# Performance work log

Measured on AMD Instinct MI355X. Metric: run time of the kernel, lower is better.

Reference implementation:

```python
import jax, jax.numpy as jnp
import numpy as np

DIM = 128  # matches init kwarg `dim`; scale = 1/sqrt(dim)


def setup_inputs() -> dict:
    key = jax.random.key(0)
    kq, kk, kv = jax.random.split(key, 3)
    B, S, D = 16, 2048, 128
    return {
        "query": jax.random.normal(kq, (B, S, D), dtype=jnp.float32),
        "key": jax.random.normal(kk, (B, S, D), dtype=jnp.float32),
        "value": jax.random.normal(kv, (B, S, D), dtype=jnp.float32),
    }


def reference(query, key, value):
    # scores = Q K^T / sqrt(dim)  -> [B, S, S]
    scale = 1.0 / np.sqrt(DIM).astype(np.float32)
    scores = jnp.einsum("bqd,bkd->bqk", query, key) * scale
    attn = jax.nn.softmax(scores, axis=-1)
    # context = attn @ V -> [B, S, D]
    return jnp.einsum("bqk,bkd->bqd", attn, value)
```

## Files before the change

kernel.cpp:

```cpp
#include <hip/hip_runtime.h>
#include <hip/hip_bf16.h>

namespace {

constexpr int kS  = 2048;
constexpr int kD  = 128;
constexpr int kKB = 128;
constexpr int kNT = kS / kKB;
constexpr int kChunks = 2048;
constexpr size_t kImgUShorts = (size_t)16 * 16 * kChunks * 8;

typedef __attribute__((ext_vector_type(8)))  short bf16x8;
typedef __attribute__((ext_vector_type(16))) float f32x16;
typedef __attribute__((ext_vector_type(4)))  unsigned int u32x4;

__device__ inline unsigned short f2bf(float f) {
  return __builtin_bit_cast(unsigned short, __float2bfloat16(f));
}
__device__ inline unsigned pk2(float lo, float hi) {
  return (unsigned)f2bf(lo) | ((unsigned)f2bf(hi) << 16);
}
__device__ inline float fexp2(float x) { return __builtin_amdgcn_exp2f(x); }

__device__ inline void gload_lds16(const void* g, void* l) {
  __builtin_amdgcn_global_load_lds(
      (const __attribute__((address_space(1))) unsigned int*)g,
      (__attribute__((address_space(3))) unsigned int*)l, 16, 0, 0);
}

__global__ __launch_bounds__(256)
void convert_kv(const float* __restrict__ K, const float* __restrict__ V,
                unsigned short* __restrict__ Kws, unsigned short* __restrict__ Vws)
{
  const int tid = threadIdx.x;
  const int gid = blockIdx.x & 255;
  const int b = gid >> 4, t = gid & 15;
  if (blockIdx.x < 256) {
    const float* src = K + ((size_t)b * kS + t * kKB) * kD;
    unsigned short* dst = Kws + (size_t)gid * kChunks * 8;
#pragma unroll
    for (int i = 0; i < 8; ++i) {
      const int CH = i * 256 + tid;
      const int k = CH >> 4, s = CH & 15;
      const int d8 = s ^ (k & 15);
      const float* p = src + (size_t)k * kD + d8 * 8;
      float4 a = *reinterpret_cast<const float4*>(p);
      float4 c = *reinterpret_cast<const float4*>(p + 4);
      bf16x8 o;
      o[0] = (short)f2bf(a.x); o[1] = (short)f2bf(a.y);
      o[2] = (short)f2bf(a.z); o[3] = (short)f2bf(a.w);
      o[4] = (short)f2bf(c.x); o[5] = (short)f2bf(c.y);
      o[6] = (short)f2bf(c.z); o[7] = (short)f2bf(c.w);
      *reinterpret_cast<bf16x8*>(dst + (size_t)CH * 8) = o;
    }
  } else {
    __shared__ unsigned short VT[128 * 136];
    const float* src = V + ((size_t)b * kS + t * kKB) * kD;
#pragma unroll
    for (int i = 0; i < 16; ++i) {
      const int idx = i * 256 + tid;
      const int k = idx >> 5, d4 = idx & 31;
      float4 v = *reinterpret_cast<const float4*>(src + (size_t)k * kD + d4 * 4);
      VT[(d4 * 4 + 0) * 136 + k] = f2bf(v.x);
      VT[(d4 * 4 + 1) * 136 + k] = f2bf(v.y);
      VT[(d4 * 4 + 2) * 136 + k] = f2bf(v.z);
      VT[(d4 * 4 + 3) * 136 + k] = f2bf(v.w);
    }
    __syncthreads();
    unsigned short* dst = Vws + (size_t)gid * kChunks * 8;
#pragma unroll
    for (int i = 0; i < 8; ++i) {
      const int CH = i * 256 + tid;
      const int d = CH >> 4, s = CH & 15;
      const int k8 = s ^ (d & 15);
      bf16x8 v = *reinterpret_cast<const bf16x8*>(&VT[d * 136 + k8 * 8]);
      *reinterpret_cast<bf16x8*>(dst + (size_t)CH * 8) = v;
    }
  }
}

__global__ __launch_bounds__(512, 2)
void attn_fwd(const float* __restrict__ Q,
              const unsigned short* __restrict__ Kws,
              const unsigned short* __restrict__ Vws,
              float* __restrict__ O)
{
  __shared__ __align__(16) unsigned char smem[131072];
  __shared__ float mls[4 * 2 * 32];

  const int tid  = threadIdx.x;
  const int wv   = tid >> 6;
  const int qg   = wv & 3;
  const int ksp  = wv >> 2;
  const int lane = tid & 63;
  const int l31  = lane & 31;
  const int hi   = lane >> 5;
  const int m15  = l31 & 15;

  const int bid   = blockIdx.x;
  const int xcd   = bid & 7;
  const int slot  = bid >> 3;
  const int batch = xcd * 2 + (slot >> 4);
  const int qtile = slot & 15;

  const float* Qb = Q + (size_t)batch * kS * kD;
  float*       Ob = O + (size_t)batch * kS * kD;
  const int qrow0 = qtile * 128 + qg * 32;

  auto stageK = [&](int t, int buf) {
    const size_t base = ((size_t)(batch * 16 + t) * kChunks + wv * 256 + lane) * 8;
    unsigned char* kd = smem + buf * 32768 + wv * 4096;
    gload_lds16(Kws + base,           kd);
    gload_lds16(Kws + base + 64 * 8,  kd + 1024);
    gload_lds16(Kws + base + 128 * 8, kd + 2048);
    gload_lds16(Kws + base + 192 * 8, kd + 3072);
  };
  auto stageV = [&](int t, int buf) {
    const size_t base = ((size_t)(batch * 16 + t) * kChunks + wv * 256 + lane) * 8;
    unsigned char* vd = smem + 65536 + buf * 32768 + wv * 4096;
    gload_lds16(Vws + base,           vd);
    gload_lds16(Vws + base + 64 * 8,  vd + 1024);
    gload_lds16(Vws + base + 128 * 8, vd + 2048);
    gload_lds16(Vws + base + 192 * 8, vd + 3072);
  };

  stageK(0, 0); stageV(0, 0); stageK(1, 1);

  constexpr float kQScale = 0.08838834764831845f * 1.4426950408889634f;
  bf16x8 qf[8];
#pragma unroll
  for (int c = 0; c < 8; ++c) {
    const float* p = Qb + (size_t)(qrow0 + l31) * kD + c * 16 + hi * 8;
    float4 a = *reinterpret_cast<const float4*>(p);
    float4 b = *reinterpret_cast<const float4*>(p + 4);
    bf16x8 f;
    f[0] = (short)f2bf(a.x * kQScale); f[1] = (short)f2bf(a.y * kQScale);
    f[2] = (short)f2bf(a.z * kQScale); f[3] = (short)f2bf(a.w * kQScale);
    f[4] = (short)f2bf(b.x * kQScale); f[5] = (short)f2bf(b.y * kQScale);
    f[6] = (short)f2bf(b.z * kQScale); f[7] = (short)f2bf(b.w * kQScale);
    qf[c] = f;
  }

  f32x16 acc[4];
#pragma unroll
  for (int dt = 0; dt < 4; ++dt)
#pragma unroll
    for (int r = 0; r < 16; ++r) acc[dt][r] = 0.f;
  float mrun = -1e30f, lrun = 0.f;
  bf16x8 pa[2][2];

  __syncthreads();

  const unsigned short* Ksm = reinterpret_cast<const unsigned short*>(smem);
  const unsigned short* Vsm = reinterpret_cast<const unsigned short*>(smem + 65536);

  auto qk = [&](int kb, f32x16 sc[2]) {
#pragma unroll
    for (int kt = 0; kt < 2; ++kt)
#pragma unroll
      for (int r = 0; r < 16; ++r) sc[kt][r] = 0.f;
    __builtin_amdgcn_s_setprio(1);
#pragma unroll
    for (int c = 0; c < 8; ++c) {
      const int s = ((c << 1) | hi) ^ m15;
#pragma unroll
      for (int kt = 0; kt < 2; ++kt) {
        const int row = ksp * 64 + kt * 32 + l31;
        bf16x8 kf = *reinterpret_cast<const bf16x8*>(&Ksm[kb * 16384 + row * 128 + s * 8]);
        sc[kt] = __builtin_amdgcn_mfma_f32_32x32x16_bf16(kf, qf[c], sc[kt], 0, 0, 0);
      }
    }
    __builtin_amdgcn_s_setprio(0);
  };
  auto treemax = [&](const f32x16 sc[2]) {
    float m0 = sc[0][0];
#pragma unroll
    for (int r = 1; r < 16; ++r) m0 = fmaxf(m0, sc[0][r]);
#pragma unroll
    for (int r = 0; r < 16; ++r) m0 = fmaxf(m0, sc[1][r]);
    return fmaxf(m0, __shfl_xor(m0, 32));
  };
  auto pv = [&](int vb) {
    __builtin_amdgcn_s_setprio(1);
#pragma unroll
    for (int dt = 0; dt < 4; ++dt) {
      const int vRow = vb * 16384 + (dt * 32 + l31) * 128;
#pragma unroll
      for (int kt = 0; kt < 2; ++kt)
#pragma unroll
        for (int ks = 0; ks < 2; ++ks) {
          const int o = 8 * ksp + 4 * kt + 2 * ks + hi;
          bf16x8 vf = *reinterpret_cast<const bf16x8*>(&Vsm[vRow + (o ^ m15) * 8]);
          acc[dt] = __builtin_amdgcn_mfma_f32_32x32x16_bf16(vf, pa[kt][ks], acc[dt], 0, 0, 0);
        }
    }
    __builtin_amdgcn_s_setprio(0);
  };
  auto pack = [&](const f32x16& p, bf16x8* out) {
    unsigned a0 = pk2(p[0], p[1]),   a1 = pk2(p[2],  p[3]);
    unsigned a2 = pk2(p[4], p[5]),   a3 = pk2(p[6],  p[7]);
    unsigned b0 = pk2(p[8], p[9]),   b1 = pk2(p[10], p[11]);
    unsigned b2 = pk2(p[12], p[13]), b3 = pk2(p[14], p[15]);
    asm("v_permlane32_swap_b32 %0, %1" : "+v"(a0), "+v"(a2));
    asm("v_permlane32_swap_b32 %0, %1" : "+v"(a1), "+v"(a3));
    asm("v_permlane32_swap_b32 %0, %1" : "+v"(b0), "+v"(b2));
    asm("v_permlane32_swap_b32 %0, %1" : "+v"(b1), "+v"(b3));
    u32x4 w0 = {a0, a1, a2, a3};
    u32x4 w1 = {b0, b1, b2, b3};
    out[0] = __builtin_bit_cast(bf16x8, w0);
    out[1] = __builtin_bit_cast(bf16x8, w1);
  };

  {
    f32x16 sc[2];
    qk(0, sc);
    mrun = treemax(sc);
    float rs = 0.f;
#pragma unroll
    for (int kt = 0; kt < 2; ++kt)
#pragma unroll
      for (int r = 0; r < 16; ++r) { sc[kt][r] = fexp2(sc[kt][r] - mrun); rs += sc[kt][r]; }
    rs += __shfl_xor(rs, 32);
    lrun = rs;
    pack(sc[0], pa[0]);
    pack(sc[1], pa[1]);
  }
  __syncthreads();

  for (int t = 0; t < kNT - 1; ++t) {
    const int kb = (t + 1) & 1, vb = t & 1;
    if (t + 2 < kNT) stageK(t + 2, vb);
    stageV(t + 1, kb);

    f32x16 sc[2];
    qk(kb, sc);
    const float mt = treemax(sc);
    const bool need = !__all(mt - mrun <= 8.0f);
    const float mnew = need ? fmaxf(mrun, mt) : mrun;

    pv(vb);

    float rs = 0.f;
#pragma unroll
    for (int kt = 0; kt < 2; ++kt)
#pragma unroll
      for (int r = 0; r < 16; ++r) { sc[kt][r] = fexp2(sc[kt][r] - mnew); rs += sc[kt][r]; }
    rs += __shfl_xor(rs, 32);
    if (need) {
      const float corr = fexp2(mrun - mnew);
      lrun *= corr;
#pragma unroll
      for (int dt = 0; dt < 4; ++dt)
#pragma unroll
        for (int r = 0; r < 16; ++r) acc[dt][r] *= corr;
    }
    lrun += rs;
    mrun = mnew;
    pack(sc[0], pa[0]);
    pack(sc[1], pa[1]);

    __syncthreads();
  }

  pv((kNT - 1) & 1);
  __syncthreads();

  float* scr = reinterpret_cast<float*>(smem);
  auto scrAt = [&](int reg, int q, int d) -> float& {
    return scr[reg * 4096 + q * 128 + (d ^ ((q & 7) << 2))];
  };
  auto drow = [&](int r) { return (r & 3) + 8 * (r >> 2) + 4 * hi; };

  if (ksp == 1) {
#pragma unroll
    for (int dt = 0; dt < 4; ++dt)
#pragma unroll
      for (int r = 0; r < 16; ++r)
        scrAt(qg, l31, dt * 32 + drow(r)) = acc[dt][r];
    mls[(qg * 2 + 0) * 32 + l31] = mrun;
    mls[(qg * 2 + 1) * 32 + l31] = lrun;
  }
  __syncthreads();
  if (ksp == 0) {
    const float m2 = mls[(qg * 2 + 0) * 32 + l31];
    const float l2 = mls[(qg * 2 + 1) * 32 + l31];
    const float mm = fmaxf(mrun, m2);
    const float w1 = fexp2(mrun - mm), w2 = fexp2(m2 - mm);
    const float inv = 1.0f / (lrun * w1 + l2 * w2);
#pragma unroll
    for (int dt = 0; dt < 4; ++dt)
#pragma unroll
      for (int r = 0; r < 16; ++r) {
        const int d = dt * 32 + drow(r);
        float o1 = scrAt(qg, l31, d);
        scrAt(qg, l31, d) = (acc[dt][r] * w1 + o1 * w2) * inv;
      }
  }
  __syncthreads();
  const int krow = tid >> 5, c4 = tid & 31;
#pragma unroll
  for (int i = 0; i < 8; ++i) {
    const int row = i * 16 + krow;
    const int q = row & 31;
    float4 val = *reinterpret_cast<const float4*>(
        &scr[(row >> 5) * 4096 + q * 128 + ((c4 * 4) ^ ((q & 7) << 2))]);
    *reinterpret_cast<float4*>(&Ob[(size_t)(qtile * 128 + row) * kD + c4 * 4]) = val;
  }
}

}

extern "C" void kernel_launch(void* const* d_in, const int* in_sizes, int n_in,
                              void* d_out, int out_size, void* d_ws, size_t ws_size,
                              hipStream_t stream) {
  const float* Q = (const float*)d_in[0];
  const float* K = (const float*)d_in[1];
  const float* V = (const float*)d_in[2];
  float* O = (float*)d_out;
  (void)in_sizes; (void)n_in; (void)out_size; (void)ws_size;

  unsigned short* Kws = (unsigned short*)d_ws;
  unsigned short* Vws = Kws + kImgUShorts;

  hipLaunchKernelGGL(convert_kv, dim3(512), dim3(256), 0, stream, K, V, Kws, Vws);
  hipLaunchKernelGGL(attn_fwd,   dim3(256), dim3(512), 0, stream, Q, Kws, Vws, O);
}
```

Measured before the change: 65.11 us.

## Halve attention tiles to 64 queries by 64 keys with 256-thread blocks

The query tile per block shrinks from 128 to 64 rows and the key/value tile from 128 to 64. Blocks drop to 4 waves (2 query groups by 2 key splits) and half the LDS, and the grid doubles to 512 blocks so more blocks fit per CU. The convert kernel and the swizzle are rewritten for the 64-key tile layout. In exchange, each K/V tile is reused by fewer query rows, so global traffic for K/V per output rises, and the loop runs twice as many iterations with a barrier and rescale check each.

```diff
diff --git a/kernel.cpp b/kernel.cpp
--- a/kernel.cpp
+++ b/kernel.cpp
@@ -5,10 +5,10 @@
 
 constexpr int kS  = 2048;
 constexpr int kD  = 128;
-constexpr int kKB = 128;
+constexpr int kKB = 64;
 constexpr int kNT = kS / kKB;
-constexpr int kChunks = 2048;
-constexpr size_t kImgUShorts = (size_t)16 * 16 * kChunks * 8;
+constexpr int kTileUS = 1024 * 8;
+constexpr size_t kImgUShorts = (size_t)16 * 32 * kTileUS;
 
 typedef __attribute__((ext_vector_type(8)))  short bf16x8;
 typedef __attribute__((ext_vector_type(16))) float f32x16;
@@ -33,13 +33,13 @@
                 unsigned short* __restrict__ Kws, unsigned short* __restrict__ Vws)
 {
   const int tid = threadIdx.x;
-  const int gid = blockIdx.x & 255;
-  const int b = gid >> 4, t = gid & 15;
-  if (blockIdx.x < 256) {
+  const int gid = blockIdx.x & 511;
+  const int b = gid >> 5, t = gid & 31;
+  if (blockIdx.x < 512) {
     const float* src = K + ((size_t)b * kS + t * kKB) * kD;
-    unsigned short* dst = Kws + (size_t)gid * kChunks * 8;
-#pragma unroll
-    for (int i = 0; i < 8; ++i) {
+    unsigned short* dst = Kws + (size_t)gid * kTileUS;
+#pragma unroll
+    for (int i = 0; i < 4; ++i) {
       const int CH = i * 256 + tid;
       const int k = CH >> 4, s = CH & 15;
       const int d8 = s ^ (k & 15);
@@ -54,74 +54,75 @@
       *reinterpret_cast<bf16x8*>(dst + (size_t)CH * 8) = o;
     }
   } else {
-    __shared__ unsigned short VT[128 * 136];
+    __shared__ unsigned short VT[128 * 72];
     const float* src = V + ((size_t)b * kS + t * kKB) * kD;
 #pragma unroll
-    for (int i = 0; i < 16; ++i) {
+    for (int i = 0; i < 8; ++i) {
       const int idx = i * 256 + tid;
       const int k = idx >> 5, d4 = idx & 31;
       float4 v = *reinterpret_cast<const float4*>(src + (size_t)k * kD + d4 * 4);
-      VT[(d4 * 4 + 0) * 136 + k] = f2bf(v.x);
-      VT[(d4 * 4 + 1) * 136 + k] = f2bf(v.y);
-      VT[(d4 * 4 + 2) * 136 + k] = f2bf(v.z);
-      VT[(d4 * 4 + 3) * 136 + k] = f2bf(v.w);
+      VT[(d4 * 4 + 0) * 72 + k] = f2bf(v.x);
+      VT[(d4 * 4 + 1) * 72 + k] = f2bf(v.y);
+      VT[(d4 * 4 + 2) * 72 + k] = f2bf(v.z);
+      VT[(d4 * 4 + 3) * 72 + k] = f2bf(v.w);
     }
     __syncthreads();
-    unsigned short* dst = Vws + (size_t)gid * kChunks * 8;
-#pragma unroll
-    for (int i = 0; i < 8; ++i) {
+    unsigned short* dst = Vws + (size_t)gid * kTileUS;
+#pragma unroll
+    for (int i = 0; i < 4; ++i) {
       const int CH = i * 256 + tid;
-      const int d = CH >> 4, s = CH & 15;
-      const int k8 = s ^ (d & 15);
-      bf16x8 v = *reinterpret_cast<const bf16x8*>(&VT[d * 136 + k8 * 8]);
+      const int d = CH >> 3, s = CH & 7;
+      const int k8 = s ^ (d & 7);
+      bf16x8 v = *reinterpret_cast<const bf16x8*>(&VT[d * 72 + k8 * 8]);
       *reinterpret_cast<bf16x8*>(dst + (size_t)CH * 8) = v;
     }
   }
 }
 
-__global__ __launch_bounds__(512, 2)
+__global__ __launch_bounds__(256, 2)
 void attn_fwd(const float* __restrict__ Q,
               const unsigned short* __restrict__ Kws,
               const unsigned short* __restrict__ Vws,
               float* __restrict__ O)
 {
-  __shared__ __align__(16) unsigned char smem[131072];
-  __shared__ float mls[4 * 2 * 32];
+  __shared__ __align__(16) unsigned char smem[65536];
+  __shared__ float mls[2 * 2 * 32];
 
   const int tid  = threadIdx.x;
   const int wv   = tid >> 6;
-  const int qg   = wv & 3;
-  const int ksp  = wv >> 2;
+  const int qg   = wv >> 1;
+  const int ksp  = wv & 1;
   const int lane = tid & 63;
   const int l31  = lane & 31;
   const int hi   = lane >> 5;
   const int m15  = l31 & 15;
+  const int m7   = l31 & 7;
 
   const int bid   = blockIdx.x;
   const int xcd   = bid & 7;
   const int slot  = bid >> 3;
-  const int batch = xcd * 2 + (slot >> 4);
-  const int qtile = slot & 15;
+  const int batch = xcd * 2 + (slot >> 5);
+  const int qt    = slot & 31;
 
   const float* Qb = Q + (size_t)batch * kS * kD;
   float*       Ob = O + (size_t)batch * kS * kD;
-  const int qrow0 = qtile * 128 + qg * 32;
+  const int qrow0 = qt * 64 + qg * 32;
 
   auto stageK = [&](int t, int buf) {
-    const size_t base = ((size_t)(batch * 16 + t) * kChunks + wv * 256 + lane) * 8;
-    unsigned char* kd = smem + buf * 32768 + wv * 4096;
-    gload_lds16(Kws + base,           kd);
-    gload_lds16(Kws + base + 64 * 8,  kd + 1024);
-    gload_lds16(Kws + base + 128 * 8, kd + 2048);
-    gload_lds16(Kws + base + 192 * 8, kd + 3072);
+    const unsigned short* src = Kws + (size_t)(batch * 32 + t) * kTileUS + (wv * 256 + lane) * 8;
+    unsigned char* kd = smem + buf * 16384 + wv * 4096;
+    gload_lds16(src,            kd);
+    gload_lds16(src + 64 * 8,   kd + 1024);
+    gload_lds16(src + 128 * 8,  kd + 2048);
+    gload_lds16(src + 192 * 8,  kd + 3072);
   };
   auto stageV = [&](int t, int buf) {
-    const size_t base = ((size_t)(batch * 16 + t) * kChunks + wv * 256 + lane) * 8;
-    unsigned char* vd = smem + 65536 + buf * 32768 + wv * 4096;
-    gload_lds16(Vws + base,           vd);
-    gload_lds16(Vws + base + 64 * 8,  vd + 1024);
-    gload_lds16(Vws + base + 128 * 8, vd + 2048);
-    gload_lds16(Vws + base + 192 * 8, vd + 3072);
+    const unsigned short* src = Vws + (size_t)(batch * 32 + t) * kTileUS + (wv * 256 + lane) * 8;
+    unsigned char* vd = smem + 32768 + buf * 16384 + wv * 4096;
+    gload_lds16(src,            vd);
+    gload_lds16(src + 64 * 8,   vd + 1024);
+    gload_lds16(src + 128 * 8,  vd + 2048);
+    gload_lds16(src + 192 * 8,  vd + 3072);
   };
 
   stageK(0, 0); stageV(0, 0); stageK(1, 1);
@@ -147,56 +148,48 @@
 #pragma unroll
     for (int r = 0; r < 16; ++r) acc[dt][r] = 0.f;
   float mrun = -1e30f, lrun = 0.f;
-  bf16x8 pa[2][2];
+  bf16x8 pa0, pa1;
 
   __syncthreads();
 
   const unsigned short* Ksm = reinterpret_cast<const unsigned short*>(smem);
-  const unsigned short* Vsm = reinterpret_cast<const unsigned short*>(smem + 65536);
-
-  auto qk = [&](int kb, f32x16 sc[2]) {
-#pragma unroll
-    for (int kt = 0; kt < 2; ++kt)
-#pragma unroll
-      for (int r = 0; r < 16; ++r) sc[kt][r] = 0.f;
+  const unsigned short* Vsm = reinterpret_cast<const unsigned short*>(smem + 32768);
+  const int kRowBase = (ksp * 32 + l31) * 128;
+
+  auto qk = [&](int kb) -> f32x16 {
+    f32x16 sc;
+#pragma unroll
+    for (int r = 0; r < 16; ++r) sc[r] = 0.f;
     __builtin_amdgcn_s_setprio(1);
 #pragma unroll
     for (int c = 0; c < 8; ++c) {
       const int s = ((c << 1) | hi) ^ m15;
-#pragma unroll
-      for (int kt = 0; kt < 2; ++kt) {
-        const int row = ksp * 64 + kt * 32 + l31;
-        bf16x8 kf = *reinterpret_cast<const bf16x8*>(&Ksm[kb * 16384 + row * 128 + s * 8]);
-        sc[kt] = __builtin_amdgcn_mfma_f32_32x32x16_bf16(kf, qf[c], sc[kt], 0, 0, 0);
-      }
+      bf16x8 kf = *reinterpret_cast<const bf16x8*>(&Ksm[kb * 8192 + kRowBase + s * 8]);
+      sc = __builtin_amdgcn_mfma_f32_32x32x16_bf16(kf, qf[c], sc, 0, 0, 0);
     }
     __builtin_amdgcn_s_setprio(0);
-  };
-  auto treemax = [&](const f32x16 sc[2]) {
-    float m0 = sc[0][0];
-#pragma unroll
-    for (int r = 1; r < 16; ++r) m0 = fmaxf(m0, sc[0][r]);
-#pragma unroll
-    for (int r = 0; r < 16; ++r) m0 = fmaxf(m0, sc[1][r]);
+    return sc;
+  };
+  auto treemax = [&](const f32x16& sc) {
+    float m0 = sc[0];
+#pragma unroll
+    for (int r = 1; r < 16; ++r) m0 = fmaxf(m0, sc[r]);
     return fmaxf(m0, __shfl_xor(m0, 32));
   };
   auto pv = [&](int vb) {
+    const int o0 = (ksp << 2) | hi;
     __builtin_amdgcn_s_setprio(1);
 #pragma unroll
     for (int dt = 0; dt < 4; ++dt) {
-      const int vRow = vb * 16384 + (dt * 32 + l31) * 128;
-#pragma unroll
-      for (int kt = 0; kt < 2; ++kt)
-#pragma unroll
-        for (int ks = 0; ks < 2; ++ks) {
-          const int o = 8 * ksp + 4 * kt + 2 * ks + hi;
-          bf16x8 vf = *reinterpret_cast<const bf16x8*>(&Vsm[vRow + (o ^ m15) * 8]);
-          acc[dt] = __builtin_amdgcn_mfma_f32_32x32x16_bf16(vf, pa[kt][ks], acc[dt], 0, 0, 0);
-        }
+      const int vRow = vb * 8192 + (dt * 32 + l31) * 64;
+      bf16x8 vf0 = *reinterpret_cast<const bf16x8*>(&Vsm[vRow + (o0 ^ m7) * 8]);
+      acc[dt] = __builtin_amdgcn_mfma_f32_32x32x16_bf16(vf0, pa0, acc[dt], 0, 0, 0);
+      bf16x8 vf1 = *reinterpret_cast<const bf16x8*>(&Vsm[vRow + ((o0 ^ 2) ^ m7) * 8]);
+      acc[dt] = __builtin_amdgcn_mfma_f32_32x32x16_bf16(vf1, pa1, acc[dt], 0, 0, 0);
     }
     __builtin_amdgcn_s_setprio(0);
   };
-  auto pack = [&](const f32x16& p, bf16x8* out) {
+  auto pack = [&](const f32x16& p) {
     unsigned a0 = pk2(p[0], p[1]),   a1 = pk2(p[2],  p[3]);
     unsigned a2 = pk2(p[4], p[5]),   a3 = pk2(p[6],  p[7]);
     unsigned b0 = pk2(p[8], p[9]),   b1 = pk2(p[10], p[11]);
@@ -207,23 +200,19 @@
     asm("v_permlane32_swap_b32 %0, %1" : "+v"(b1), "+v"(b3));
     u32x4 w0 = {a0, a1, a2, a3};
     u32x4 w1 = {b0, b1, b2, b3};
-    out[0] = __builtin_bit_cast(bf16x8, w0);
-    out[1] = __builtin_bit_cast(bf16x8, w1);
+    pa0 = __builtin_bit_cast(bf16x8, w0);
+    pa1 = __builtin_bit_cast(bf16x8, w1);
   };
 
   {
-    f32x16 sc[2];
-    qk(0, sc);
+    f32x16 sc = qk(0);
     mrun = treemax(sc);
     float rs = 0.f;
 #pragma unroll
-    for (int kt = 0; kt < 2; ++kt)
-#pragma unroll
-      for (int r = 0; r < 16; ++r) { sc[kt][r] = fexp2(sc[kt][r] - mrun); rs += sc[kt][r]; }
+    for (int r = 0; r < 16; ++r) { sc[r] = fexp2(sc[r] - mrun); rs += sc[r]; }
     rs += __shfl_xor(rs, 32);
     lrun = rs;
-    pack(sc[0], pa[0]);
-    pack(sc[1], pa[1]);
+    pack(sc);
   }
   __syncthreads();
 
@@ -232,8 +221,7 @@
     if (t + 2 < kNT) stageK(t + 2, vb);
     stageV(t + 1, kb);
 
-    f32x16 sc[2];
-    qk(kb, sc);
+    f32x16 sc = qk(kb);
     const float mt = treemax(sc);
     const bool need = !__all(mt - mrun <= 8.0f);
     const float mnew = need ? fmaxf(mrun, mt) : mrun;
@@ -242,9 +230,7 @@
 
     float rs = 0.f;
 #pragma unroll
-    for (int kt = 0; kt < 2; ++kt)
-#pragma unroll
-      for (int r = 0; r < 16; ++r) { sc[kt][r] = fexp2(sc[kt][r] - mnew); rs += sc[kt][r]; }
+    for (int r = 0; r < 16; ++r) { sc[r] = fexp2(sc[r] - mnew); rs += sc[r]; }
     rs += __shfl_xor(rs, 32);
     if (need) {
       const float corr = fexp2(mrun - mnew);
@@ -256,8 +242,7 @@
     }
     lrun += rs;
     mrun = mnew;
-    pack(sc[0], pa[0]);
-    pack(sc[1], pa[1]);
+    pack(sc);
 
     __syncthreads();
   }
@@ -300,11 +285,11 @@
   const int krow = tid >> 5, c4 = tid & 31;
 #pragma unroll
   for (int i = 0; i < 8; ++i) {
-    const int row = i * 16 + krow;
+    const int row = i * 8 + krow;
     const int q = row & 31;
     float4 val = *reinterpret_cast<const float4*>(
         &scr[(row >> 5) * 4096 + q * 128 + ((c4 * 4) ^ ((q & 7) << 2))]);
-    *reinterpret_cast<float4*>(&Ob[(size_t)(qtile * 128 + row) * kD + c4 * 4]) = val;
+    *reinterpret_cast<float4*>(&Ob[(size_t)(qt * 64 + row) * kD + c4 * 4]) = val;
   }
 }
 
@@ -322,6 +307,6 @@
   unsigned short* Kws = (unsigned short*)d_ws;
   unsigned short* Vws = Kws + kImgUShorts;
 
-  hipLaunchKernelGGL(convert_kv, dim3(512), dim3(256), 0, stream, K, V, Kws, Vws);
-  hipLaunchKernelGGL(attn_fwd,   dim3(256), dim3(512), 0, stream, Q, Kws, Vws, O);
-}
+  hipLaunchKernelGGL(convert_kv, dim3(1024), dim3(256), 0, stream, K, V, Kws, Vws);
+  hipLaunchKernelGGL(attn_fwd,   dim3(512),  dim3(256), 0, stream, Q, Kws, Vws, O);
+}
```

New measurement: 69.51 us. +6.8%, slower.
